# Kernel tuning notes

Hardware: AMD Instinct MI355X
Metric: run time of the kernel (lower is better)

The kernel has to match this reference:

```python
import jax, jax.numpy as jnp
import numpy as np

# ---- ANI symmetry-function constants (from __init__ defaults) ----
N_ATOMS = 50000
N_ELEMENTS = 7
RADIAL_CUTOFF = 5.1      # angstrom
ANGULAR_CUTOFF = 3.5     # angstrom
RADIAL_START = 0.8
ANGULAR_START = 0.8
RADIAL_DIV = 8           # radial_sublength = 8
ANGULAR_DIV = 8
ANGLE_SECTIONS = 4       # angular sublength = 4*8 = 32
ETA_R = 19.7
ETA_A = 12.5
ZETA = 14.1

ShfR = np.linspace(RADIAL_START, RADIAL_CUTOFF, RADIAL_DIV + 1, dtype=np.float32)[:-1]
ShfA = np.linspace(ANGULAR_START, ANGULAR_CUTOFF, ANGULAR_DIV + 1, dtype=np.float32)[:-1]
ShfZ = ((np.arange(ANGLE_SECTIONS, dtype=np.float32) + 0.5) * np.pi / ANGLE_SECTIONS)


def cosine_cutoff(d, rc):
    return jnp.where(d <= rc, 0.5 * jnp.cos(jnp.pi * d / rc) + 0.5, 0.0)


def setup_inputs() -> dict:
    key = jax.random.key(0)
    k1, k2, k3, k4, k5 = jax.random.split(key, 5)
    n_pairs, n_trip = 1_600_000, 1_600_000
    # pair distances in [0.8, 5.1)
    r_ij = jax.random.uniform(k1, (n_pairs,), jnp.float32) * (RADIAL_CUTOFF - RADIAL_START) + RADIAL_START
    pair_indices = jax.random.randint(k2, (2, n_pairs), 0, N_ATOMS, jnp.int32)
    atomic_numbers = jax.random.randint(k3, (N_ATOMS,), 0, N_ELEMENTS, jnp.int32)
    # triplet displacement vectors with norms in [0.8, 3.5)
    dirs = jax.random.normal(k4, (2, n_trip, 3), jnp.float32)
    dirs = dirs / jnp.linalg.norm(dirs, axis=-1, keepdims=True)
    mags = jax.random.uniform(k5, (2, n_trip, 1), jnp.float32) * (ANGULAR_CUTOFF - ANGULAR_START) + ANGULAR_START
    vec12 = dirs * mags
    return {"r_ij": r_ij, "pair_indices": pair_indices,
            "atomic_numbers": atomic_numbers, "vec12": vec12}


def _radial_features(d):
    # [P, 8]: ANI radial symmetry function
    fc = cosine_cutoff(d, RADIAL_CUTOFF)
    g = 0.25 * jnp.exp(-ETA_R * (d[:, None] - jnp.asarray(ShfR)) ** 2)
    return g * fc[:, None]


def _angular_features(vec12):
    v1, v2 = vec12[0], vec12[1]                       # [T, 3]
    d1 = jnp.linalg.norm(v1, axis=-1)
    d2 = jnp.linalg.norm(v2, axis=-1)
    cos_t = 0.95 * jnp.sum(v1 * v2, axis=-1) / (d1 * d2)
    theta = jnp.arccos(cos_t)                         # [T]
    f_ang = ((1.0 + jnp.cos(theta[:, None] - jnp.asarray(ShfZ))) * 0.5) ** ZETA   # [T, 4]
    f_rad = jnp.exp(-ETA_A * (0.5 * (d1 + d2)[:, None] - jnp.asarray(ShfA)) ** 2) # [T, 8]
    fc = cosine_cutoff(d1, ANGULAR_CUTOFF) * cosine_cutoff(d2, ANGULAR_CUTOFF)    # [T]
    ang = 2.0 * f_ang[:, :, None] * f_rad[:, None, :] * fc[:, None, None]          # [T, 4, 8]
    return ang.reshape(ang.shape[0], ANGLE_SECTIONS * ANGULAR_DIV)                 # [T, 32]


def reference(r_ij, pair_indices, atomic_numbers, vec12):
    # radial branch
    feat = _radial_features(r_ij)                     # [P, 8]
    species12 = atomic_numbers[pair_indices]          # [2, P]
    index12 = pair_indices * N_ELEMENTS + species12[::-1]  # flip(0): use partner species
    aev = jnp.zeros((N_ATOMS * N_ELEMENTS, RADIAL_DIV), feat.dtype)
    aev = aev.at[index12[0]].add(feat).at[index12[1]].add(feat)
    # angular branch
    ang = _angular_features(vec12)                    # [T, 32]
    return (aev, ang)
```

## Files before the change

kernel.cpp:

```cpp
#include <hip/hip_runtime.h>


#define N_ATOMS 50000
#define N_ELEM 7
#define RADIAL_DIV 8
#define NROWS (N_ATOMS * N_ELEM)

constexpr float RADIAL_CUTOFF = 5.1f;
constexpr float ANGULAR_CUTOFF = 3.5f;
constexpr float ETA_R = 19.7f;
constexpr float ETA_A = 12.5f;
constexpr float ZETA = 14.1f;
constexpr float PI_F = 3.14159265358979323846f;
constexpr float FP_SCALE = 4096.0f;
constexpr float FP_INV = 1.0f / 4096.0f;
constexpr float SHELL_STEP = 0.5375f;
constexpr float INV_SHELL_STEP = 1.0f / 0.5375f;

__device__ __constant__ float CSZ[4] = { 0.9238795325f,  0.3826834324f, -0.3826834324f, -0.9238795325f };
__device__ __constant__ float SNZ[4] = { 0.3826834324f,  0.9238795325f,  0.9238795325f,  0.3826834324f };

#define BLK 256

typedef __attribute__((ext_vector_type(4))) float f4;

__global__ __launch_bounds__(BLK) void fused_kernel(
        const float* __restrict__ r_ij,
        const int* __restrict__ pair_idx,
        const int* __restrict__ Z,
        unsigned long long* __restrict__ acc,
        int P,
        const float* __restrict__ vec12,
        float* __restrict__ ang,
        int T,
        int nRad, int nAng) {
    __shared__ float sm[BLK * 33];
    int bid = blockIdx.x;
    int tid = threadIdx.x;

    int fullG = (min(nRad, nAng)) >> 3;
    int base = fullG * 16;
    bool isAng;
    int id;
    if (bid < base) {
        int grp = bid >> 3;
        isAng = ((grp & 1) == 0);
        id = (grp >> 1) * 8 + (bid & 7);
    } else {
        int l = bid - base;
        int angLeft = nAng - fullG * 8;
        if (l < angLeft) { isAng = true;  id = fullG * 8 + l; }
        else             { isAng = false; id = fullG * 8 + (l - angLeft); }
    }

    if (!isAng) {
        int t = id * BLK + tid;
        if (t >= P) return;
        float d = __builtin_nontemporal_load(r_ij + t);
        float fc = (d <= RADIAL_CUTOFF)
                       ? (0.5f * __cosf(PI_F * d * (1.0f / RADIAL_CUTOFF)) + 0.5f)
                       : 0.0f;

        float x = (d - 0.8f) * INV_SHELL_STEP;
        int k0 = (int)(x + 0.5f);
        k0 = min(max(k0, 1), 6);
        int a = k0 - 1;
        int g = a >> 1;
        int sh = (a & 1) << 4;

        unsigned long long w = 0ull;
        #pragma unroll
        for (int j = 0; j < 3; j++) {
            float diff = d - (0.8f + SHELL_STEP * (float)(a + j));
            float gv = 0.25f * __expf(-ETA_R * diff * diff) * fc;
            unsigned int q = (unsigned int)(gv * FP_SCALE + 0.5f);
            w |= (unsigned long long)q << (16 * j);
        }
        w <<= sh;
        if (w == 0ull) return;

        int i0 = __builtin_nontemporal_load(pair_idx + t);
        int i1 = __builtin_nontemporal_load(pair_idx + P + t);
        int s0 = Z[i0];
        int s1 = Z[i1];
        atomicAdd(acc + ((size_t)i0 * N_ELEM + s1) * 3 + g, w);
        atomicAdd(acc + ((size_t)i1 * N_ELEM + s0) * 3 + g, w);
        return;
    }

    int t = id * BLK + tid;
    float vals[32];
    if (t < T) {
        const float* v1 = vec12 + 3ull * (size_t)t;
        const float* v2 = vec12 + 3ull * (size_t)T + 3ull * (size_t)t;
        float x1 = __builtin_nontemporal_load(v1 + 0);
        float y1 = __builtin_nontemporal_load(v1 + 1);
        float z1 = __builtin_nontemporal_load(v1 + 2);
        float x2 = __builtin_nontemporal_load(v2 + 0);
        float y2 = __builtin_nontemporal_load(v2 + 1);
        float z2 = __builtin_nontemporal_load(v2 + 2);

        float d1 = sqrtf(x1 * x1 + y1 * y1 + z1 * z1);
        float d2 = sqrtf(x2 * x2 + y2 * y2 + z2 * z2);
        float dot = x1 * x2 + y1 * y2 + z1 * z2;
        float cost = 0.95f * dot / (d1 * d2);
        float sint = sqrtf(fmaxf(0.0f, 1.0f - cost * cost));

        float fc1 = (d1 <= ANGULAR_CUTOFF) ? (0.5f * __cosf(PI_F * d1 * (1.0f / ANGULAR_CUTOFF)) + 0.5f) : 0.0f;
        float fc2 = (d2 <= ANGULAR_CUTOFF) ? (0.5f * __cosf(PI_F * d2 * (1.0f / ANGULAR_CUTOFF)) + 0.5f) : 0.0f;
        float fc = fc1 * fc2;

        float davg = 0.5f * (d1 + d2);
        float frad[8];
        #pragma unroll
        for (int k = 0; k < 8; k++) {
            float diff = davg - (0.8f + 0.3375f * (float)k);
            frad[k] = __expf(-ETA_A * diff * diff);
        }
        #pragma unroll
        for (int j = 0; j < 4; j++) {
            float c = 0.5f * (1.0f + cost * CSZ[j] + sint * SNZ[j]);
            float base2 = 2.0f * __powf(c, ZETA) * fc;
            #pragma unroll
            for (int k = 0; k < 8; k++) vals[j * 8 + k] = base2 * frad[k];
        }
    } else {
        #pragma unroll
        for (int k = 0; k < 32; k++) vals[k] = 0.0f;
    }

    #pragma unroll
    for (int k = 0; k < 32; k++) sm[tid * 33 + k] = vals[k];
    __syncthreads();

    size_t obase = (size_t)id * BLK * 32;
    size_t lim = (size_t)T * 32;
    #pragma unroll
    for (int it = 0; it < 8; it++) {
        int f = it * BLK + tid;
        int row = f >> 3;
        int col = (f & 7) * 4;
        f4 o;
        o.x = sm[row * 33 + col + 0];
        o.y = sm[row * 33 + col + 1];
        o.z = sm[row * 33 + col + 2];
        o.w = sm[row * 33 + col + 3];
        size_t gidx = obase + (size_t)f * 4;
        if (gidx < lim)
            __builtin_nontemporal_store(o, reinterpret_cast<f4*>(ang) + (gidx >> 2));
    }
}

__global__ void convert_kernel(const unsigned long long* __restrict__ acc,
                               float* __restrict__ aev, int nrows) {
    int r = blockIdx.x * blockDim.x + threadIdx.x;
    if (r >= nrows) return;
    unsigned long long g0 = acc[3 * (size_t)r + 0];
    unsigned long long g1 = acc[3 * (size_t)r + 1];
    unsigned long long g2 = acc[3 * (size_t)r + 2];
    unsigned int l0[4], l1[4], l2[4];
    #pragma unroll
    for (int j = 0; j < 4; j++) {
        l0[j] = (unsigned int)(g0 >> (16 * j)) & 0xFFFFu;
        l1[j] = (unsigned int)(g1 >> (16 * j)) & 0xFFFFu;
        l2[j] = (unsigned int)(g2 >> (16 * j)) & 0xFFFFu;
    }
    f4 oa, ob;
    oa.x = (float)(l0[0])         * FP_INV;
    oa.y = (float)(l0[1])         * FP_INV;
    oa.z = (float)(l0[2] + l1[0]) * FP_INV;
    oa.w = (float)(l0[3] + l1[1]) * FP_INV;
    ob.x = (float)(l1[2] + l2[0]) * FP_INV;
    ob.y = (float)(l1[3] + l2[1]) * FP_INV;
    ob.z = (float)(l2[2])         * FP_INV;
    ob.w = (float)(l2[3])         * FP_INV;
    f4* o = reinterpret_cast<f4*>(aev + 8ull * (size_t)r);
    __builtin_nontemporal_store(oa, o + 0);
    __builtin_nontemporal_store(ob, o + 1);
}

extern "C" void kernel_launch(void* const* d_in, const int* in_sizes, int n_in,
                              void* d_out, int out_size, void* d_ws, size_t ws_size,
                              hipStream_t stream) {
    const float* r_ij     = (const float*)d_in[0];
    const int*   pair_idx = (const int*)d_in[1];
    const int*   Z        = (const int*)d_in[2];
    const float* vec12    = (const float*)d_in[3];

    const int P = in_sizes[0];
    const int T = in_sizes[3] / 6;

    float* aev = (float*)d_out;
    float* ang = aev + (size_t)NROWS * RADIAL_DIV;

    unsigned long long* acc = (unsigned long long*)d_ws;
    hipMemsetAsync(acc, 0, (size_t)NROWS * 3 * sizeof(unsigned long long), stream);

    const int nRad = (P + BLK - 1) / BLK;
    const int nAng = (T + BLK - 1) / BLK;
    fused_kernel<<<dim3(nRad + nAng), dim3(BLK), 0, stream>>>(
        r_ij, pair_idx, Z, acc, P, vec12, ang, T, nRad, nAng);
    convert_kernel<<<dim3((NROWS + 255) / 256), dim3(256), 0, stream>>>(acc, aev, NROWS);
}
```

Baseline: 375.3 us.

## Replicate radial accumulators per XCD with workgroup-scope atomics

```diff
diff --git a/kernel.cpp b/kernel.cpp
--- a/kernel.cpp
+++ b/kernel.cpp
@@ -24,6 +24,7 @@
 
 typedef __attribute__((ext_vector_type(4))) float f4;
 
+template <bool XCD_REP>
 __global__ __launch_bounds__(BLK) void fused_kernel(
         const float* __restrict__ r_ij,
         const int* __restrict__ pair_idx,
@@ -83,8 +84,19 @@
         int i1 = __builtin_nontemporal_load(pair_idx + P + t);
         int s0 = Z[i0];
         int s1 = Z[i1];
-        atomicAdd(acc + ((size_t)i0 * N_ELEM + s1) * 3 + g, w);
-        atomicAdd(acc + ((size_t)i1 * N_ELEM + s0) * 3 + g, w);
+        size_t o0 = ((size_t)i0 * N_ELEM + s1) * 3 + g;
+        size_t o1 = ((size_t)i1 * N_ELEM + s0) * 3 + g;
+
+        if constexpr (XCD_REP) {
+            unsigned int xcc;
+            asm("s_getreg_b32 %0, hwreg(HW_REG_XCC_ID)" : "=s"(xcc));
+            unsigned long long* accr = acc + (size_t)(xcc & 7u) * ((size_t)NROWS * 3);
+            __hip_atomic_fetch_add(accr + o0, w, __ATOMIC_RELAXED, __HIP_MEMORY_SCOPE_WORKGROUP);
+            __hip_atomic_fetch_add(accr + o1, w, __ATOMIC_RELAXED, __HIP_MEMORY_SCOPE_WORKGROUP);
+        } else {
+            atomicAdd(acc + o0, w);
+            atomicAdd(acc + o1, w);
+        }
         return;
     }
 
@@ -152,18 +164,23 @@
 }
 
 __global__ void convert_kernel(const unsigned long long* __restrict__ acc,
-                               float* __restrict__ aev, int nrows) {
+                               float* __restrict__ aev, int nrows, int R) {
     int r = blockIdx.x * blockDim.x + threadIdx.x;
     if (r >= nrows) return;
-    unsigned long long g0 = acc[3 * (size_t)r + 0];
-    unsigned long long g1 = acc[3 * (size_t)r + 1];
-    unsigned long long g2 = acc[3 * (size_t)r + 2];
-    unsigned int l0[4], l1[4], l2[4];
-    #pragma unroll
-    for (int j = 0; j < 4; j++) {
-        l0[j] = (unsigned int)(g0 >> (16 * j)) & 0xFFFFu;
-        l1[j] = (unsigned int)(g1 >> (16 * j)) & 0xFFFFu;
-        l2[j] = (unsigned int)(g2 >> (16 * j)) & 0xFFFFu;
+    unsigned int l0[4] = {0, 0, 0, 0};
+    unsigned int l1[4] = {0, 0, 0, 0};
+    unsigned int l2[4] = {0, 0, 0, 0};
+    for (int rep = 0; rep < R; rep++) {
+        const unsigned long long* a = acc + (size_t)rep * nrows * 3 + 3 * (size_t)r;
+        unsigned long long g0 = a[0];
+        unsigned long long g1 = a[1];
+        unsigned long long g2 = a[2];
+        #pragma unroll
+        for (int j = 0; j < 4; j++) {
+            l0[j] += (unsigned int)(g0 >> (16 * j)) & 0xFFFFu;
+            l1[j] += (unsigned int)(g1 >> (16 * j)) & 0xFFFFu;
+            l2[j] += (unsigned int)(g2 >> (16 * j)) & 0xFFFFu;
+        }
     }
     f4 oa, ob;
     oa.x = (float)(l0[0])         * FP_INV;
@@ -193,12 +210,21 @@
     float* aev = (float*)d_out;
     float* ang = aev + (size_t)NROWS * RADIAL_DIV;
 
+    const size_t repBytes = (size_t)NROWS * 3 * sizeof(unsigned long long);
+    const bool xcdRep = (ws_size >= 8 * repBytes);
+    const int R = xcdRep ? 8 : 1;
+
     unsigned long long* acc = (unsigned long long*)d_ws;
-    hipMemsetAsync(acc, 0, (size_t)NROWS * 3 * sizeof(unsigned long long), stream);
+    hipMemsetAsync(acc, 0, (size_t)R * repBytes, stream);
 
     const int nRad = (P + BLK - 1) / BLK;
     const int nAng = (T + BLK - 1) / BLK;
-    fused_kernel<<<dim3(nRad + nAng), dim3(BLK), 0, stream>>>(
-        r_ij, pair_idx, Z, acc, P, vec12, ang, T, nRad, nAng);
-    convert_kernel<<<dim3((NROWS + 255) / 256), dim3(256), 0, stream>>>(acc, aev, NROWS);
+    if (xcdRep) {
+        fused_kernel<true><<<dim3(nRad + nAng), dim3(BLK), 0, stream>>>(
+            r_ij, pair_idx, Z, acc, P, vec12, ang, T, nRad, nAng);
+    } else {
+        fused_kernel<false><<<dim3(nRad + nAng), dim3(BLK), 0, stream>>>(
+            r_ij, pair_idx, Z, acc, P, vec12, ang, T, nRad, nAng);
+    }
+    convert_kernel<<<dim3((NROWS + 255) / 256), dim3(256), 0, stream>>>(acc, aev, NROWS, R);
 }
```

New measurement: 406.6 us. +8.3%, slower.
